# Performance work log

Measured on AMD Instinct MI355X. Metric: run time of the kernel, lower is better.

The kernel has to match this reference:

```python
import jax, jax.numpy as jnp
import numpy as np

N_EMBD = 1024
NUM_HEADS = 16
HEAD_SIZE = N_EMBD // NUM_HEADS
B, T = 2, 2048


def setup_inputs() -> dict:
    key = jax.random.key(0)
    k1, k2, k3, k4 = jax.random.split(key, 4)
    x = jax.random.normal(k1, (B, T, N_EMBD), dtype=jnp.float32)
    # torch nn.Linear weight is [out,in]; we store transposed [in,out] for x @ W
    w_qkv = jax.random.normal(k2, (N_EMBD, 3 * N_EMBD), dtype=jnp.float32) * (N_EMBD ** -0.5)
    w_proj = jax.random.normal(k3, (N_EMBD, N_EMBD), dtype=jnp.float32) * (N_EMBD ** -0.5)
    b_proj = jax.random.normal(k4, (N_EMBD,), dtype=jnp.float32) * 0.01
    return {"x": x, "w_qkv": w_qkv, "w_proj": w_proj, "b_proj": b_proj}


def reference(x, w_qkv, w_proj, b_proj):
    Bm, Tm, C = x.shape
    H, D = NUM_HEADS, HEAD_SIZE
    qkv = x @ w_qkv  # [B,T,3C]
    # einops 'b t (h d three) -> three b h t d': 'three' is the innermost factor
    qkv = qkv.reshape(Bm, Tm, H, D, 3)
    q = qkv[..., 0].transpose(0, 2, 1, 3)  # [B,H,T,D]
    k = qkv[..., 1].transpose(0, 2, 1, 3)
    v = qkv[..., 2].transpose(0, 2, 1, 3)
    scale = D ** -0.5
    attn = jnp.einsum('bhqd,bhkd->bhqk', q, k) * scale  # [B,H,T,T]
    causal_mask = jnp.triu(jnp.ones((Tm, Tm), dtype=bool), k=1)
    attn = jnp.where(causal_mask, -jnp.inf, attn)
    attn = jax.nn.softmax(attn, axis=-1)
    out = jnp.einsum('bhqk,bhkd->bhqd', attn, v)  # [B,H,T,D]
    out = out.transpose(0, 2, 1, 3).reshape(Bm, Tm, C)  # b h t d -> b t (h d)
    out = out @ w_proj + b_proj
    return out
```

## Files before the change

### kernel.cpp

```cpp
#include <hip/hip_runtime.h>
#include <hip/hip_bf16.h>
#include <math.h>

typedef __bf16 bf16x8 __attribute__((ext_vector_type(8)));
typedef __bf16 bf16x4 __attribute__((ext_vector_type(4)));
typedef float f32x4 __attribute__((ext_vector_type(4)));

#define MFMA16(A, B, C) __builtin_amdgcn_mfma_f32_16x16x32_bf16(A, B, C, 0, 0, 0)

__device__ __forceinline__ void cp16(void* lds_base, const void* g) {
  __builtin_amdgcn_global_load_lds(
      (const __attribute__((address_space(1))) void*)g,
      (__attribute__((address_space(3))) void*)lds_base, 16, 0, 0);
}

static constexpr int Bc   = 2;
static constexpr int Tc   = 2048;
static constexpr int Cc   = 1024;
static constexpr int Hc   = 16;
static constexpr int Dc   = 64;
static constexpr int Mrows = Bc * Tc;
static constexpr int N3    = 3 * Cc;

__global__ __launch_bounds__(256) void convert_x(
    const float* __restrict__ src, __bf16* __restrict__ dst, int n) {
  const int i0 = (blockIdx.x * 256 + threadIdx.x) * 8;
  if (i0 >= n) return;
  f32x4 a = *(const f32x4*)(src + i0);
  f32x4 b = *(const f32x4*)(src + i0 + 4);
  bf16x8 v;
#pragma unroll
  for (int j = 0; j < 4; ++j) { v[j] = (__bf16)a[j]; v[4 + j] = (__bf16)b[j]; }
  *(bf16x8*)(dst + i0) = v;
}

__global__ __launch_bounds__(256) void transpose_weights(
    const float* __restrict__ wqkv, const float* __restrict__ wproj,
    __bf16* __restrict__ dqkv, __bf16* __restrict__ dproj) {
  __shared__ __bf16 tile[32][33];
  const bool isproj = blockIdx.x >= 96;
  const float* src = isproj ? wproj : wqkv;
  __bf16* dst = isproj ? dproj : dqkv;
  const int N = isproj ? Cc : N3;
  const int K = Cc;
  const int n0 = (isproj ? (blockIdx.x - 96) : blockIdx.x) * 32;
  const int k0 = blockIdx.y * 32;
  const int x = threadIdx.x & 31;
  const int y = threadIdx.x >> 5;
  {
    int n = n0 + x;
    int col = n;
    if (!isproj) {
      int three = n >> 10, rem = n & 1023;
      int h = rem >> 6, d = rem & 63;
      col = h * 192 + d * 3 + three;
    }
#pragma unroll
    for (int r = 0; r < 4; ++r) {
      int k = k0 + y + r * 8;
      tile[y + r * 8][x] = (__bf16)src[(size_t)k * N + col];
    }
  }
  __syncthreads();
#pragma unroll
  for (int r = 0; r < 4; ++r) {
    int n = n0 + y + r * 8;
    dst[(size_t)n * K + k0 + x] = tile[x][y + r * 8];
  }
}

template <bool F32OUT>
__global__ __launch_bounds__(256) void gemm_nt(
    const __bf16* __restrict__ A, const __bf16* __restrict__ Bt,
    void* __restrict__ Cmat, const float* __restrict__ bias,
    int M, int N, int K, int ldc) {
  __shared__ __align__(16) __bf16 As[128 * 64];
  __shared__ __align__(16) __bf16 Bs[128 * 64];
  const int n0 = blockIdx.x * 128, m0 = blockIdx.y * 128;
  const int tid = threadIdx.x;
  const int wave = tid >> 6, lane = tid & 63;
  const int quad = lane >> 4, l16 = lane & 15;
  const int wm = (wave >> 1) * 64, wn = (wave & 1) * 64;
  const int srow = lane >> 3;
  const int scol = (((lane & 7) ^ (srow & 7))) * 8;

  f32x4 acc[4][4] = {};

  for (int k0 = 0; k0 < K; k0 += 64) {
    __syncthreads();
#pragma unroll
    for (int c = 0; c < 4; ++c) {
      int rowblk = c * 4 + wave;
      int row = rowblk * 8 + srow;
      cp16(&As[rowblk * 512], A + (size_t)(m0 + row) * K + k0 + scol);
      cp16(&Bs[rowblk * 512], Bt + (size_t)(n0 + row) * K + k0 + scol);
    }
    __syncthreads();
#pragma unroll
    for (int kk = 0; kk < 64; kk += 32) {
      bf16x8 af[4], bfr[4];
#pragma unroll
      for (int i = 0; i < 4; ++i) {
        int chunk = (((kk >> 3) + quad) ^ (l16 & 7)) * 8;
        af[i]  = *(const bf16x8*)(&As[(wm + i * 16 + l16) * 64 + chunk]);
        bfr[i] = *(const bf16x8*)(&Bs[(wn + i * 16 + l16) * 64 + chunk]);
      }
#pragma unroll
      for (int mi = 0; mi < 4; ++mi)
#pragma unroll
        for (int ni = 0; ni < 4; ++ni)
          acc[mi][ni] = MFMA16(af[mi], bfr[ni], acc[mi][ni]);
    }
  }

#pragma unroll
  for (int ni = 0; ni < 4; ++ni) {
    int col = n0 + wn + ni * 16 + l16;
    float bv = bias ? bias[col] : 0.0f;
#pragma unroll
    for (int mi = 0; mi < 4; ++mi)
#pragma unroll
      for (int r = 0; r < 4; ++r) {
        int row = m0 + wm + mi * 16 + quad * 4 + r;
        float v = acc[mi][ni][r] + bv;
        if (F32OUT)
          ((float*)Cmat)[(size_t)row * ldc + col] = v;
        else
          ((__bf16*)Cmat)[(size_t)row * ldc + col] = (__bf16)v;
      }
  }
}

__global__ __launch_bounds__(256) void gemm_qkv(
    const __bf16* __restrict__ A, const __bf16* __restrict__ Bt,
    __bf16* __restrict__ C, __bf16* __restrict__ vt,
    int M, int N, int K, int ldc) {
  __shared__ __align__(16) __bf16 sm[2][2][128 * 64];
  const int n0 = blockIdx.x * 128, m0 = blockIdx.y * 128;
  const int tid = threadIdx.x;
  const int wave = tid >> 6, lane = tid & 63;
  const int quad = lane >> 4, l16 = lane & 15;
  const int wm = (wave >> 1) * 64, wn = (wave & 1) * 64;
  const int srow = lane >> 3;
  const int scol = (((lane & 7) ^ (srow & 7))) * 8;
  const int NT = K >> 6;

  f32x4 acc[4][4] = {};

  const __bf16* Abase = A + (size_t)m0 * K;
  const __bf16* Bbase = Bt + (size_t)n0 * K;

  auto stage = [&](int t) {
    __bf16* dstA = &sm[t & 1][0][0];
    __bf16* dstB = &sm[t & 1][1][0];
    const int koff = t * 64 + scol;
#pragma unroll
    for (int c = 0; c < 4; ++c) {
      int rowblk = c * 4 + wave;
      int row = rowblk * 8 + srow;
      cp16(dstA + rowblk * 512, Abase + (size_t)row * K + koff);
      cp16(dstB + rowblk * 512, Bbase + (size_t)row * K + koff);
    }
  };

  stage(0);
  stage(1);

  for (int t = 0; t < NT; ++t) {
    if (t + 1 < NT)
      asm volatile("s_waitcnt vmcnt(8)" ::: "memory");
    else
      asm volatile("s_waitcnt vmcnt(0)" ::: "memory");
    __builtin_amdgcn_s_barrier();
    asm volatile("" ::: "memory");

    const __bf16* As_ = &sm[t & 1][0][0];
    const __bf16* Bs_ = &sm[t & 1][1][0];
#pragma unroll
    for (int kk = 0; kk < 64; kk += 32) {
      bf16x8 af[4], bfr[4];
#pragma unroll
      for (int i = 0; i < 4; ++i) {
        int chunk = (((kk >> 3) + quad) ^ (l16 & 7)) * 8;
        af[i]  = *(const bf16x8*)(&As_[(wm + i * 16 + l16) * 64 + chunk]);
        bfr[i] = *(const bf16x8*)(&Bs_[(wn + i * 16 + l16) * 64 + chunk]);
      }
      __builtin_amdgcn_s_setprio(1);
#pragma unroll
      for (int mi = 0; mi < 4; ++mi)
#pragma unroll
        for (int ni = 0; ni < 4; ++ni)
          acc[mi][ni] = MFMA16(af[mi], bfr[ni], acc[mi][ni]);
      __builtin_amdgcn_s_setprio(0);
    }

    asm volatile("" ::: "memory");
    __builtin_amdgcn_s_barrier();
    if (t + 2 < NT) stage(t + 2);
  }

  if (n0 < 2 * Cc) {
#pragma unroll
    for (int ni = 0; ni < 4; ++ni) {
      int col = n0 + wn + ni * 16 + l16;
#pragma unroll
      for (int mi = 0; mi < 4; ++mi)
#pragma unroll
        for (int r = 0; r < 4; ++r) {
          int row = m0 + wm + mi * 16 + quad * 4 + r;
          C[(size_t)row * ldc + col] = (__bf16)acc[mi][ni][r];
        }
    }
  } else {
    constexpr int LPT = 136;
    __bf16* tr = &sm[0][0][0];
    __builtin_amdgcn_s_barrier();
#pragma unroll
    for (int ni = 0; ni < 4; ++ni) {
      int collocal = wn + ni * 16 + l16;
#pragma unroll
      for (int mi = 0; mi < 4; ++mi) {
        int row0 = wm + mi * 16 + quad * 4;
        bf16x4 ov;
#pragma unroll
        for (int r = 0; r < 4; ++r) ov[r] = (__bf16)acc[mi][ni][r];
        *(bf16x4*)(&tr[collocal * LPT + row0]) = ov;
      }
    }
    __syncthreads();
    const int hdl = tid >> 1, half = tid & 1;
    const int hdg = (n0 - 2 * Cc) + hdl;
    const int h = hdg >> 6, d = hdg & 63;
    const int bb = m0 >> 11, tt0 = (m0 & 2047) + half * 64;
    __bf16* dstrow = vt + ((size_t)(bb * Hc + h) * Dc + d) * Tc + tt0;
    const __bf16* srcrow = &tr[hdl * LPT + half * 64];
#pragma unroll
    for (int j = 0; j < 8; ++j)
      *(bf16x8*)(dstrow + j * 8) = *(const bf16x8*)(srcrow + j * 8);
  }
}

#define LOG2E 1.44269504088896340736f
#define C2SC  (0.125f * LOG2E)
#define SH2   (16.0f * LOG2E)
static constexpr int LPK = 72;
static constexpr int LPV = 136;
static constexpr int TB  = 128;

__global__ __launch_bounds__(512, 4) void attn_kernel(
    const __bf16* __restrict__ qkv,
    const __bf16* __restrict__ vt,
    __bf16* __restrict__ obuf) {
  __shared__ __align__(16) __bf16 Ks[TB * LPK];
  __shared__ __align__(16) __bf16 Vs[64 * LPV];
  __shared__ __align__(16) __bf16 plds[8][16 * LPK];

  const int bh = blockIdx.x;
  const int torder = blockIdx.y;
  const int qt = (torder < 8) ? torder : (23 - torder);
  const int q0 = qt * 128;
  const int b = bh >> 4, hh = bh & 15;
  const int tid = threadIdx.x;
  const int wave = tid >> 6, lane = tid & 63;
  const int quad = lane >> 4, l16 = lane & 15;
  const int qb = q0 + wave * 16;
  const int kblocks = q0 + 128;

  const __bf16* qbase = qkv + (size_t)(b * Tc) * N3 + hh * 64;
  const __bf16* kbase = qbase + Cc;
  const __bf16* vtb = vt + (size_t)bh * 64 * Tc;

  const int krow = tid >> 2;
  const int kcol = (tid & 3) * 16;
  const int vrow = tid >> 3;
  const int vcol = (tid & 7) * 16;

  bf16x8 bQ[2];
  {
    const __bf16* qr = qbase + (size_t)(qb + l16) * N3;
    bQ[0] = *(const bf16x8*)(qr + quad * 8);
    bQ[1] = *(const bf16x8*)(qr + 32 + quad * 8);
  }

  f32x4 accO[4] = {};
  float l_part = 0.0f;

  bf16x8 kp[2], vp[2];
  {
    const __bf16* kr = kbase + (size_t)krow * N3 + kcol;
    const __bf16* vr = vtb + (size_t)vrow * Tc + vcol;
#pragma unroll
    for (int j = 0; j < 2; ++j) {
      kp[j] = *(const bf16x8*)(kr + j * 8);
      vp[j] = *(const bf16x8*)(vr + j * 8);
    }
  }

  for (int kc = 0; kc < kblocks; kc += TB) {
    __syncthreads();
#pragma unroll
    for (int j = 0; j < 2; ++j) {
      *(bf16x8*)(&Ks[krow * LPK + kcol + j * 8]) = kp[j];
      *(bf16x8*)(&Vs[vrow * LPV + vcol + j * 8]) = vp[j];
    }
    if (kc + TB < kblocks) {
      const __bf16* kr = kbase + (size_t)(kc + TB + krow) * N3 + kcol;
      const __bf16* vr = vtb + (size_t)vrow * Tc + kc + TB + vcol;
#pragma unroll
      for (int j = 0; j < 2; ++j) {
        kp[j] = *(const bf16x8*)(kr + j * 8);
        vp[j] = *(const bf16x8*)(vr + j * 8);
      }
    }
    __syncthreads();

#pragma unroll
    for (int sub = 0; sub < 2; ++sub) {
      const int kc2 = kc + sub * 64;
      if (kc2 >= qb + 16) continue;

      f32x4 st[4];
#pragma unroll
      for (int kt = 0; kt < 4; ++kt) {
        const int trow = sub * 64 + kt * 16 + l16;
        bf16x8 kf0 = *(const bf16x8*)(&Ks[trow * LPK + quad * 8]);
        bf16x8 kf1 = *(const bf16x8*)(&Ks[trow * LPK + 32 + quad * 8]);
        f32x4 a = {};
        a = MFMA16(kf0, bQ[0], a);
        a = MFMA16(kf1, bQ[1], a);
        st[kt] = a;
      }
      if (kc2 + 64 > qb) {
        int qcol = qb + l16;
#pragma unroll
        for (int kt = 0; kt < 4; ++kt)
#pragma unroll
          for (int r = 0; r < 4; ++r) {
            int t = kc2 + kt * 16 + quad * 4 + r;
            if (t > qcol) st[kt][r] = -INFINITY;
          }
      }
#pragma unroll
      for (int kt = 0; kt < 4; ++kt)
#pragma unroll
        for (int r = 0; r < 4; ++r) {
          float p = __builtin_amdgcn_exp2f(fmaf(st[kt][r], C2SC, -SH2));
          st[kt][r] = p;
          l_part += p;
        }
#pragma unroll
      for (int kt = 0; kt < 4; ++kt) {
        bf16x4 pv;
#pragma unroll
        for (int r = 0; r < 4; ++r) pv[r] = (__bf16)st[kt][r];
        *(bf16x4*)(&plds[wave][l16 * LPK + kt * 16 + quad * 4]) = pv;
      }
      __threadfence_block();
      bf16x8 bP[2];
      bP[0] = *(const bf16x8*)(&plds[wave][l16 * LPK + quad * 8]);
      bP[1] = *(const bf16x8*)(&plds[wave][l16 * LPK + 32 + quad * 8]);
#pragma unroll
      for (int dt = 0; dt < 4; ++dt) {
        const int drow = (dt * 16 + l16) * LPV + sub * 64;
        bf16x8 vf0 = *(const bf16x8*)(&Vs[drow + quad * 8]);
        bf16x8 vf1 = *(const bf16x8*)(&Vs[drow + 32 + quad * 8]);
        accO[dt] = MFMA16(vf0, bP[0], accO[dt]);
        accO[dt] = MFMA16(vf1, bP[1], accO[dt]);
      }
    }
  }

  {
    float l_i = l_part;
    l_i += __shfl_xor(l_i, 16);
    l_i += __shfl_xor(l_i, 32);
    float inv = 1.0f / l_i;
    __bf16* orow = obuf + (size_t)(b * Tc + qb + l16) * Cc + hh * 64;
#pragma unroll
    for (int dt = 0; dt < 4; ++dt) {
      bf16x4 ov;
#pragma unroll
      for (int r = 0; r < 4; ++r) ov[r] = (__bf16)(accO[dt][r] * inv);
      *(bf16x4*)(orow + dt * 16 + quad * 4) = ov;
    }
  }
}

extern "C" void kernel_launch(void* const* d_in, const int* in_sizes, int n_in,
                              void* d_out, int out_size, void* d_ws, size_t ws_size,
                              hipStream_t stream) {
  const float* x      = (const float*)d_in[0];
  const float* w_qkv  = (const float*)d_in[1];
  const float* w_proj = (const float*)d_in[2];
  const float* b_proj = (const float*)d_in[3];

  bool f32out = true;
  {
    size_t out_bytes = 0;
    if (hipMemPtrGetInfo(d_out, &out_bytes) == hipSuccess && out_bytes != 0)
      f32out = out_bytes >= (size_t)out_size * 4;
  }

  __bf16* xb     = (__bf16*)d_ws;
  __bf16* wqkvT  = xb + (size_t)Mrows * Cc;
  __bf16* wprojT = wqkvT + (size_t)N3 * Cc;
  __bf16* qkvp   = wprojT + (size_t)Cc * Cc;
  __bf16* vt     = qkvp + (size_t)Mrows * N3;
  __bf16* obuf   = vt + (size_t)Bc * Hc * Dc * Tc;

  convert_x<<<(Mrows * Cc) / (256 * 8), 256, 0, stream>>>(x, xb, Mrows * Cc);
  transpose_weights<<<dim3(128, 32), 256, 0, stream>>>(
      w_qkv, w_proj, wqkvT, wprojT);
  gemm_qkv<<<dim3(N3 / 128, Mrows / 128), 256, 0, stream>>>(
      xb, wqkvT, qkvp, vt, Mrows, N3, Cc, N3);
  attn_kernel<<<dim3(Bc * Hc, 16), 512, 0, stream>>>(qkvp, vt, obuf);
  if (f32out) {
    gemm_nt<true><<<dim3(Cc / 128, Mrows / 128), 256, 0, stream>>>(
        obuf, wprojT, d_out, b_proj, Mrows, Cc, Cc, Cc);
  } else {
    gemm_nt<false><<<dim3(Cc / 128, Mrows / 128), 256, 0, stream>>>(
        obuf, wprojT, d_out, b_proj, Mrows, Cc, Cc, Cc);
  }
}
```

Before: 173.1 us.

## Double-buffer LDS in projection GEMM with async prefetch and MFMA priority

The projection GEMM now keeps two LDS stages and prefetches tile t+2 while computing tile t. It uses explicit vmcnt waits and raw barriers in place of two full syncthreads per iteration. The MFMA section is also raised in priority with s_setprio. This targets global-load latency in a small output GEMM at the cost of doubled LDS use (64KB), which may reduce occupancy.

```diff
diff --git a/kernel.cpp b/kernel.cpp
--- a/kernel.cpp
+++ b/kernel.cpp
@@ -70,12 +70,11 @@
 }
 
 template <bool F32OUT>
-__global__ __launch_bounds__(256) void gemm_nt(
+__global__ __launch_bounds__(256) void gemm_proj(
     const __bf16* __restrict__ A, const __bf16* __restrict__ Bt,
     void* __restrict__ Cmat, const float* __restrict__ bias,
     int M, int N, int K, int ldc) {
-  __shared__ __align__(16) __bf16 As[128 * 64];
-  __shared__ __align__(16) __bf16 Bs[128 * 64];
+  __shared__ __align__(16) __bf16 sm[2][2][128 * 64];
   const int n0 = blockIdx.x * 128, m0 = blockIdx.y * 128;
   const int tid = threadIdx.x;
   const int wave = tid >> 6, lane = tid & 63;
@@ -83,34 +82,60 @@
   const int wm = (wave >> 1) * 64, wn = (wave & 1) * 64;
   const int srow = lane >> 3;
   const int scol = (((lane & 7) ^ (srow & 7))) * 8;
+  const int NT = K >> 6;
 
   f32x4 acc[4][4] = {};
 
-  for (int k0 = 0; k0 < K; k0 += 64) {
-    __syncthreads();
+  const __bf16* Abase = A + (size_t)m0 * K;
+  const __bf16* Bbase = Bt + (size_t)n0 * K;
+
+  auto stage = [&](int t) {
+    __bf16* dstA = &sm[t & 1][0][0];
+    __bf16* dstB = &sm[t & 1][1][0];
+    const int koff = t * 64 + scol;
 #pragma unroll
     for (int c = 0; c < 4; ++c) {
       int rowblk = c * 4 + wave;
       int row = rowblk * 8 + srow;
-      cp16(&As[rowblk * 512], A + (size_t)(m0 + row) * K + k0 + scol);
-      cp16(&Bs[rowblk * 512], Bt + (size_t)(n0 + row) * K + k0 + scol);
-    }
-    __syncthreads();
+      cp16(dstA + rowblk * 512, Abase + (size_t)row * K + koff);
+      cp16(dstB + rowblk * 512, Bbase + (size_t)row * K + koff);
+    }
+  };
+
+  stage(0);
+  stage(1);
+
+  for (int t = 0; t < NT; ++t) {
+    if (t + 1 < NT)
+      asm volatile("s_waitcnt vmcnt(8)" ::: "memory");
+    else
+      asm volatile("s_waitcnt vmcnt(0)" ::: "memory");
+    __builtin_amdgcn_s_barrier();
+    asm volatile("" ::: "memory");
+
+    const __bf16* As_ = &sm[t & 1][0][0];
+    const __bf16* Bs_ = &sm[t & 1][1][0];
 #pragma unroll
     for (int kk = 0; kk < 64; kk += 32) {
       bf16x8 af[4], bfr[4];
 #pragma unroll
       for (int i = 0; i < 4; ++i) {
         int chunk = (((kk >> 3) + quad) ^ (l16 & 7)) * 8;
-        af[i]  = *(const bf16x8*)(&As[(wm + i * 16 + l16) * 64 + chunk]);
-        bfr[i] = *(const bf16x8*)(&Bs[(wn + i * 16 + l16) * 64 + chunk]);
-      }
+        af[i]  = *(const bf16x8*)(&As_[(wm + i * 16 + l16) * 64 + chunk]);
+        bfr[i] = *(const bf16x8*)(&Bs_[(wn + i * 16 + l16) * 64 + chunk]);
+      }
+      __builtin_amdgcn_s_setprio(1);
 #pragma unroll
       for (int mi = 0; mi < 4; ++mi)
 #pragma unroll
         for (int ni = 0; ni < 4; ++ni)
           acc[mi][ni] = MFMA16(af[mi], bfr[ni], acc[mi][ni]);
-    }
+      __builtin_amdgcn_s_setprio(0);
+    }
+
+    asm volatile("" ::: "memory");
+    __builtin_amdgcn_s_barrier();
+    if (t + 2 < NT) stage(t + 2);
   }
 
 #pragma unroll
@@ -415,10 +440,10 @@
       xb, wqkvT, qkvp, vt, Mrows, N3, Cc, N3);
   attn_kernel<<<dim3(Bc * Hc, 16), 512, 0, stream>>>(qkvp, vt, obuf);
   if (f32out) {
-    gemm_nt<true><<<dim3(Cc / 128, Mrows / 128), 256, 0, stream>>>(
+    gemm_proj<true><<<dim3(Cc / 128, Mrows / 128), 256, 0, stream>>>(
         obuf, wprojT, d_out, b_proj, Mrows, Cc, Cc, Cc);
   } else {
-    gemm_nt<false><<<dim3(Cc / 128, Mrows / 128), 256, 0, stream>>>(
+    gemm_proj<false><<<dim3(Cc / 128, Mrows / 128), 256, 0, stream>>>(
         obuf, wprojT, d_out, b_proj, Mrows, Cc, Cc, Cc);
   }
 }
```

New measurement: 165.8 us. 4.2% less time.
